# Performance work log

Hardware: AMD Instinct MI355X
Metric: run time of the kernel (lower is better)

## Reference

```python
import jax, jax.numpy as jnp
import numpy as np

N_HEADS = 8
N_DIM = 512
ATTN_DIM = N_DIM // N_HEADS
SOFT_TEMPERATURE = 1.0
TEMPERATURE = ATTN_DIM ** 0.5 / SOFT_TEMPERATURE


def sparsemax(z):
    # sparsemax along last axis: euclidean projection onto the simplex
    n = z.shape[-1]
    z_sorted = -jnp.sort(-z, axis=-1)                      # descending
    cs = jnp.cumsum(z_sorted, axis=-1)
    k = jnp.arange(1, n + 1, dtype=z.dtype)
    support = 1.0 + k * z_sorted > cs                      # bool
    k_sel = jnp.sum(support, axis=-1, keepdims=True)       # support size >= 1
    cs_sel = jnp.take_along_axis(cs, k_sel - 1, axis=-1)
    tau = (cs_sel - 1.0) / k_sel.astype(z.dtype)
    return jnp.maximum(z - tau, 0.0)


def setup_inputs() -> dict:
    key = jax.random.key(0)
    ks = jax.random.split(key, 9)
    bs, L, d = 8, 1024, N_DIM
    s = 1.0 / np.sqrt(d)
    return {
        "h_q": jax.random.normal(ks[0], (bs, L, d), jnp.float32),
        "h_k": jax.random.normal(ks[1], (bs, L, d), jnp.float32),
        "h_v": jax.random.normal(ks[2], (bs, L, d), jnp.float32),
        "Wq": jax.random.normal(ks[3], (d, d), jnp.float32) * s,
        "Wk": jax.random.normal(ks[4], (d, d), jnp.float32) * s,
        "Wv": jax.random.normal(ks[5], (d, d), jnp.float32) * s,
        "bv": jax.random.normal(ks[6], (d,), jnp.float32) * s,
        "Wf": jax.random.normal(ks[7], (d, d), jnp.float32) * s,
        "bf": jax.random.normal(ks[8], (d,), jnp.float32) * s,
    }


def reference(h_q, h_k, h_v, Wq, Wk, Wv, bv, Wf, bf):
    bs, Lq, _ = h_q.shape
    Lk = h_k.shape[1]
    H, D = N_HEADS, ATTN_DIM
    q = (h_q @ Wq.T).reshape(bs, Lq, H, D).transpose(0, 2, 1, 3)   # bhqd
    k = (h_k @ Wk.T).reshape(bs, Lk, H, D).transpose(0, 2, 1, 3)   # bhkd
    v = (h_v @ Wv.T + bv).reshape(bs, Lk, H, D).transpose(0, 2, 1, 3)
    alpha = jnp.einsum('bhqd,bhkd->bhqk', q / TEMPERATURE, k)
    alpha = sparsemax(alpha)
    res = jnp.einsum('bhqk,bhkd->bhqd', alpha, v)
    res = res.transpose(0, 2, 1, 3).reshape(bs, Lq, H * D)
    return res @ Wf.T + bf
```

## Files before the change

kernel.cpp:

```cpp
#include <hip/hip_runtime.h>
#include <hip/hip_bf16.h>
#include <cstdint>
#include <cstddef>

#define BS 8
#define SEQ 1024
#define DMODEL 512
#define NHEADS 8
#define DHEAD 64
#define QBLK 16
#define PPAD 1032

typedef float f32x4 __attribute__((ext_vector_type(4)));
typedef short bf16x8 __attribute__((ext_vector_type(8)));

static __device__ __forceinline__ unsigned short f2bf(float v) {
    __hip_bfloat16 hb = __float2bfloat16(v);
    return *reinterpret_cast<unsigned short*>(&hb);
}

struct CvtJob { const float* s; unsigned short* d; int n4; };

__global__ __launch_bounds__(256) void cvt_many(
    CvtJob j0, CvtJob j1, CvtJob j2, CvtJob j3, CvtJob j4, CvtJob j5, CvtJob j6)
{
    CvtJob j;
    switch (blockIdx.y) {
        case 0: j = j0; break; case 1: j = j1; break; case 2: j = j2; break;
        case 3: j = j3; break; case 4: j = j4; break; case 5: j = j5; break;
        default: j = j6; break;
    }
    for (int i = blockIdx.x * 256 + threadIdx.x; i < j.n4; i += gridDim.x * 256) {
        const float4 f = ((const float4*)j.s)[i];
        uint2 u;
        u.x = (unsigned)f2bf(f.x) | ((unsigned)f2bf(f.y) << 16);
        u.y = (unsigned)f2bf(f.z) | ((unsigned)f2bf(f.w) << 16);
        ((uint2*)j.d)[i] = u;
    }
}

struct GArgs { const unsigned short* A; const unsigned short* W;
               const float* bias; void* C; float scale; int mode; };

__global__ __launch_bounds__(256) void gemm_mfma(GArgs g0, GArgs g1, GArgs g2) {
    __shared__ __align__(16) unsigned short As[64 * 64];
    __shared__ __align__(16) unsigned short Bs[128 * 64];

    const GArgs g = (blockIdx.z == 0) ? g0 : ((blockIdx.z == 1) ? g1 : g2);
    const int tid = threadIdx.x;
    const int w = tid >> 6, l = tid & 63, lr = l & 15, lg = l >> 4;
    const int bm = blockIdx.y * 64, bn = blockIdx.x * 128;
    const int mrow = (w & 1) * 32, ncol = (w >> 1) * 64;

    f32x4 acc[2][4];
#pragma unroll
    for (int mt = 0; mt < 2; ++mt)
#pragma unroll
        for (int nt = 0; nt < 4; ++nt) acc[mt][nt] = (f32x4)0.f;

    for (int k0 = 0; k0 < DMODEL; k0 += 64) {
#pragma unroll
        for (int i = 0; i < 2; ++i) {
            const int rbase = i * 32 + w * 8;
            const int r = rbase + (l >> 3);
            const unsigned short* src = g.A + (size_t)(bm + r) * DMODEL + k0
                                        + 8 * ((l & 7) ^ (r & 7));
            __builtin_amdgcn_global_load_lds((const unsigned int*)src,
                                             (unsigned int*)&As[rbase * 64], 16, 0, 0);
        }
#pragma unroll
        for (int i = 0; i < 4; ++i) {
            const int rbase = i * 32 + w * 8;
            const int r = rbase + (l >> 3);
            const unsigned short* src = g.W + (size_t)(bn + r) * DMODEL + k0
                                        + 8 * ((l & 7) ^ (r & 7));
            __builtin_amdgcn_global_load_lds((const unsigned int*)src,
                                             (unsigned int*)&Bs[rbase * 64], 16, 0, 0);
        }
        __syncthreads();
#pragma unroll
        for (int kk = 0; kk < 2; ++kk) {
            bf16x8 av[2], bv[4];
#pragma unroll
            for (int mt = 0; mt < 2; ++mt) {
                const int ra = mrow + mt * 16 + lr;
                av[mt] = *(const bf16x8*)&As[ra * 64 + 8 * ((kk * 4 + lg) ^ (ra & 7))];
            }
#pragma unroll
            for (int nt = 0; nt < 4; ++nt) {
                const int rb = ncol + nt * 16 + lr;
                bv[nt] = *(const bf16x8*)&Bs[rb * 64 + 8 * ((kk * 4 + lg) ^ (rb & 7))];
            }
#pragma unroll
            for (int mt = 0; mt < 2; ++mt)
#pragma unroll
                for (int nt = 0; nt < 4; ++nt)
                    acc[mt][nt] = __builtin_amdgcn_mfma_f32_16x16x32_bf16(
                        av[mt], bv[nt], acc[mt][nt], 0, 0, 0);
        }
        __syncthreads();
    }

    if (g.mode == 0) {
        float* C = (float*)g.C;
#pragma unroll
        for (int mt = 0; mt < 2; ++mt)
#pragma unroll
        for (int nt = 0; nt < 4; ++nt)
#pragma unroll
        for (int j = 0; j < 4; ++j) {
            const int r = bm + mrow + mt * 16 + lg * 4 + j;
            const int c = bn + ncol + nt * 16 + lr;
            C[(size_t)r * DMODEL + c] = acc[mt][nt][j] * g.scale
                                        + (g.bias ? g.bias[c] : 0.f);
        }
    } else if (g.mode == 1) {
        unsigned short* C = (unsigned short*)g.C;
#pragma unroll
        for (int mt = 0; mt < 2; ++mt)
#pragma unroll
        for (int nt = 0; nt < 4; ++nt)
#pragma unroll
        for (int j = 0; j < 4; ++j) {
            const int r = bm + mrow + mt * 16 + lg * 4 + j;
            const int c = bn + ncol + nt * 16 + lr;
            const float v = acc[mt][nt][j] * g.scale + (g.bias ? g.bias[c] : 0.f);
            const int b = r >> 10, ll = r & (SEQ - 1);
            const int h = c >> 6, dd = c & 63;
            C[((size_t)(b * NHEADS + h) * SEQ + ll) * DHEAD + dd] = f2bf(v);
        }
    } else {
        unsigned short* C = (unsigned short*)g.C;
#pragma unroll
        for (int mt = 0; mt < 2; ++mt)
#pragma unroll
        for (int nt = 0; nt < 4; ++nt) {
            const int c = bn + ncol + nt * 16 + lr;
            const int h = c >> 6, dd = c & 63;
            const int r0 = bm + mrow + mt * 16 + lg * 4;
            const int b = r0 >> 10, l0 = r0 & (SEQ - 1);
            unsigned short tmp[4];
#pragma unroll
            for (int j = 0; j < 4; ++j)
                tmp[j] = f2bf(acc[mt][nt][j] * g.scale + (g.bias ? g.bias[c] : 0.f));
            uint2 u;
            u.x = (unsigned)tmp[0] | ((unsigned)tmp[1] << 16);
            u.y = (unsigned)tmp[2] | ((unsigned)tmp[3] << 16);
            *(uint2*)&C[((size_t)(b * NHEADS + h) * DHEAD + dd) * SEQ + l0] = u;
        }
    }
}

__global__ __launch_bounds__(256, 4) void attn_mfma(
    const unsigned short* __restrict__ Q, const unsigned short* __restrict__ K,
    const unsigned short* __restrict__ Vt, unsigned short* __restrict__ R)
{
    __shared__ __align__(16) unsigned short P[QBLK][PPAD];
    __shared__ float red_s[2][4][QBLK];
    __shared__ float red_c[2][4][QBLK];

    const int tid = threadIdx.x;
    const int w = tid >> 6, l = tid & 63, lr = l & 15, lg = l >> 4;

    const int flat = blockIdx.x;
    const int nid = (flat & 7) * 512 + (flat >> 3);
    const int q0 = (nid & 63) * QBLK;
    const int h = (nid >> 6) & (NHEADS - 1);
    const int b = nid >> 9;

    const size_t base = (size_t)(b * NHEADS + h) * SEQ * DHEAD;
    const unsigned short* Qp = Q + base;
    const unsigned short* Kp = K + base;

    const int ks = w * 256;

    const bf16x8 aq0 = *(const bf16x8*)(Qp + (size_t)(q0 + lr) * DHEAD + lg * 8);
    const bf16x8 aq1 = *(const bf16x8*)(Qp + (size_t)(q0 + lr) * DHEAD + 32 + lg * 8);
    f32x4 acc[16];
#pragma unroll
    for (int t = 0; t < 16; ++t) acc[t] = (f32x4)0.f;
#pragma unroll
    for (int t = 0; t < 16; ++t) {
        const unsigned short* kp = Kp + (size_t)(ks + t * 16 + lr) * DHEAD + lg * 8;
        const bf16x8 bk0 = *(const bf16x8*)(kp);
        const bf16x8 bk1 = *(const bf16x8*)(kp + 32);
        acc[t] = __builtin_amdgcn_mfma_f32_16x16x32_bf16(aq0, bk0, acc[t], 0, 0, 0);
        acc[t] = __builtin_amdgcn_mfma_f32_16x16x32_bf16(aq1, bk1, acc[t], 0, 0, 0);
    }

    float mx[4];
#pragma unroll
    for (int j = 0; j < 4; ++j) mx[j] = acc[0][j];
#pragma unroll
    for (int t = 1; t < 16; ++t)
#pragma unroll
        for (int j = 0; j < 4; ++j) mx[j] = fmaxf(mx[j], acc[t][j]);
#pragma unroll
    for (int o = 1; o < 16; o <<= 1)
#pragma unroll
        for (int j = 0; j < 4; ++j) mx[j] = fmaxf(mx[j], __shfl_xor(mx[j], o));
    if (lr == 0) {
#pragma unroll
        for (int j = 0; j < 4; ++j) red_s[0][w][lg * 4 + j] = mx[j];
    }
    __syncthreads();
    float tau[4];
#pragma unroll
    for (int j = 0; j < 4; ++j) {
        const int r = lg * 4 + j;
        tau[j] = fmaxf(fmaxf(red_s[0][0][r], red_s[0][1][r]),
                       fmaxf(red_s[0][2][r], red_s[0][3][r])) - 1.0f;
    }

    for (int it = 0; it < 16; ++it) {
        const int bb = (it + 1) & 1;
        float s[4] = {0.f, 0.f, 0.f, 0.f};
        float c[4] = {0.f, 0.f, 0.f, 0.f};
#pragma unroll
        for (int t = 0; t < 16; ++t)
#pragma unroll
            for (int j = 0; j < 4; ++j) {
                const bool ggt = acc[t][j] > tau[j];
                s[j] += ggt ? acc[t][j] : 0.f;
                c[j] += ggt ? 1.f : 0.f;
            }
#pragma unroll
        for (int o = 1; o < 16; o <<= 1)
#pragma unroll
            for (int j = 0; j < 4; ++j) {
                s[j] += __shfl_xor(s[j], o);
                c[j] += __shfl_xor(c[j], o);
            }
        if (lr == 0) {
#pragma unroll
            for (int j = 0; j < 4; ++j) {
                red_s[bb][w][lg * 4 + j] = s[j];
                red_c[bb][w][lg * 4 + j] = c[j];
            }
        }
        __syncthreads();
        float delta = -1.f;
#pragma unroll
        for (int j = 0; j < 4; ++j) {
            const int r = lg * 4 + j;
            const float st = red_s[bb][0][r] + red_s[bb][1][r]
                           + red_s[bb][2][r] + red_s[bb][3][r];
            const float ct = red_c[bb][0][r] + red_c[bb][1][r]
                           + red_c[bb][2][r] + red_c[bb][3][r];
            const float tn = (st - 1.f) / ct;
            delta = fmaxf(delta, tn - tau[j]);
            tau[j] = tn;
        }
        delta = fmaxf(delta, __shfl_xor(delta, 16));
        delta = fmaxf(delta, __shfl_xor(delta, 32));
        if (delta < 1e-5f) break;
    }

#pragma unroll
    for (int t = 0; t < 16; ++t)
#pragma unroll
        for (int j = 0; j < 4; ++j)
            P[lg * 4 + j][ks + t * 16 + lr] = f2bf(fmaxf(acc[t][j] - tau[j], 0.f));
    __syncthreads();

    const int dcol = w * 16;
    const unsigned short* VtP = Vt + ((size_t)(b * NHEADS + h) * DHEAD + dcol + lr) * SEQ
                                + lg * 8;
    f32x4 o = (f32x4)0.f;
    bf16x8 vb = *(const bf16x8*)(VtP);
#pragma unroll 4
    for (int kt = 0; kt < 32; ++kt) {
        const bf16x8 vcur = vb;
        if (kt + 1 < 32) vb = *(const bf16x8*)(VtP + (kt + 1) * 32);
        const bf16x8 pa = *(const bf16x8*)&P[lr][kt * 32 + lg * 8];
        __builtin_amdgcn_s_setprio(1);
        o = __builtin_amdgcn_mfma_f32_16x16x32_bf16(pa, vcur, o, 0, 0, 0);
        __builtin_amdgcn_s_setprio(0);
    }

#pragma unroll
    for (int j = 0; j < 4; ++j)
        R[((size_t)b * SEQ + q0 + lg * 4 + j) * DMODEL + h * DHEAD + dcol + lr] =
            f2bf(o[j]);
}

extern "C" void kernel_launch(void* const* d_in, const int* in_sizes, int n_in,
                              void* d_out, int out_size, void* d_ws, size_t ws_size,
                              hipStream_t stream) {
    const float* h_q = (const float*)d_in[0];
    const float* h_k = (const float*)d_in[1];
    const float* h_v = (const float*)d_in[2];
    const float* Wq  = (const float*)d_in[3];
    const float* Wk  = (const float*)d_in[4];
    const float* Wv  = (const float*)d_in[5];
    const float* bv  = (const float*)d_in[6];
    const float* Wf  = (const float*)d_in[7];
    const float* bf  = (const float*)d_in[8];
    float* out = (float*)d_out;

    const size_t perT = (size_t)BS * SEQ * DMODEL;
    const size_t wN = (size_t)DMODEL * DMODEL;
    unsigned short* hq_b = (unsigned short*)d_ws;
    unsigned short* hk_b = hq_b + perT;
    unsigned short* hv_b = hk_b + perT;
    unsigned short* Qws  = hv_b + perT;
    unsigned short* Kws  = Qws + perT;
    unsigned short* Vtw  = Kws + perT;
    unsigned short* Rws  = Vtw + perT;
    unsigned short* Wqb  = Rws + perT;
    unsigned short* Wkb  = Wqb + wN;
    unsigned short* Wvb  = Wkb + wN;
    unsigned short* Wfb  = Wvb + wN;

    {
        CvtJob j0{h_q, hq_b, (int)(perT / 4)};
        CvtJob j1{h_k, hk_b, (int)(perT / 4)};
        CvtJob j2{h_v, hv_b, (int)(perT / 4)};
        CvtJob j3{Wq, Wqb, (int)(wN / 4)};
        CvtJob j4{Wk, Wkb, (int)(wN / 4)};
        CvtJob j5{Wv, Wvb, (int)(wN / 4)};
        CvtJob j6{Wf, Wfb, (int)(wN / 4)};
        cvt_many<<<dim3(512, 7), 256, 0, stream>>>(j0, j1, j2, j3, j4, j5, j6);
    }

    {
        GArgs gq{hq_b, Wqb, nullptr, Qws, 0.125f, 1};
        GArgs gk{hk_b, Wkb, nullptr, Kws, 1.0f, 1};
        GArgs gv{hv_b, Wvb, bv,      Vtw, 1.0f, 2};
        gemm_mfma<<<dim3(DMODEL / 128, BS * SEQ / 64, 3), 256, 0, stream>>>(gq, gk, gv);
    }

    attn_mfma<<<dim3(BS * NHEADS * (SEQ / QBLK)), 256, 0, stream>>>(Qws, Kws, Vtw, Rws);

    {
        GArgs gf{Rws, Wfb, bf, out, 1.0f, 0};
        gemm_mfma<<<dim3(DMODEL / 128, BS * SEQ / 64, 1), 256, 0, stream>>>(gf, gf, gf);
    }
}
```

Measured before the change: 190.4 us.

## Compact sparsemax candidates into shared list and transpose QK MFMA layout

```diff
diff --git a/kernel.cpp b/kernel.cpp
--- a/kernel.cpp
+++ b/kernel.cpp
@@ -156,8 +156,11 @@
     const unsigned short* __restrict__ Vt, unsigned short* __restrict__ R)
 {
     __shared__ __align__(16) unsigned short P[QBLK][PPAD];
-    __shared__ float red_s[2][4][QBLK];
-    __shared__ float red_c[2][4][QBLK];
+    __shared__ __align__(16) float clist[QBLK][68];
+    __shared__ int cnt_s[QBLK];
+    __shared__ __align__(16) float red_m[QBLK][4];
+    __shared__ __align__(16) float red_s[2][QBLK][4];
+    __shared__ __align__(16) float red_c[2][QBLK][4];
 
     const int tid = threadIdx.x;
     const int w = tid >> 6, l = tid & 63, lr = l & 15, lg = l >> 4;
@@ -184,99 +187,124 @@
         const unsigned short* kp = Kp + (size_t)(ks + t * 16 + lr) * DHEAD + lg * 8;
         const bf16x8 bk0 = *(const bf16x8*)(kp);
         const bf16x8 bk1 = *(const bf16x8*)(kp + 32);
-        acc[t] = __builtin_amdgcn_mfma_f32_16x16x32_bf16(aq0, bk0, acc[t], 0, 0, 0);
-        acc[t] = __builtin_amdgcn_mfma_f32_16x16x32_bf16(aq1, bk1, acc[t], 0, 0, 0);
-    }
-
-    float mx[4];
-#pragma unroll
-    for (int j = 0; j < 4; ++j) mx[j] = acc[0][j];
-#pragma unroll
-    for (int t = 1; t < 16; ++t)
-#pragma unroll
-        for (int j = 0; j < 4; ++j) mx[j] = fmaxf(mx[j], acc[t][j]);
-#pragma unroll
-    for (int o = 1; o < 16; o <<= 1)
-#pragma unroll
-        for (int j = 0; j < 4; ++j) mx[j] = fmaxf(mx[j], __shfl_xor(mx[j], o));
-    if (lr == 0) {
-#pragma unroll
-        for (int j = 0; j < 4; ++j) red_s[0][w][lg * 4 + j] = mx[j];
-    }
+        acc[t] = __builtin_amdgcn_mfma_f32_16x16x32_bf16(bk0, aq0, acc[t], 0, 0, 0);
+        acc[t] = __builtin_amdgcn_mfma_f32_16x16x32_bf16(bk1, aq1, acc[t], 0, 0, 0);
+    }
+
+    f32x4 m4 = acc[0];
+#pragma unroll
+    for (int t = 1; t < 16; ++t) {
+        m4[0] = fmaxf(m4[0], acc[t][0]); m4[1] = fmaxf(m4[1], acc[t][1]);
+        m4[2] = fmaxf(m4[2], acc[t][2]); m4[3] = fmaxf(m4[3], acc[t][3]);
+    }
+    float m = fmaxf(fmaxf(m4[0], m4[1]), fmaxf(m4[2], m4[3]));
+    m = fmaxf(m, __shfl_xor(m, 16));
+    m = fmaxf(m, __shfl_xor(m, 32));
+    if (lg == 0) red_m[lr][w] = m;
+
+    for (int i = tid; i < QBLK * 68; i += 256) (&clist[0][0])[i] = -3.0e38f;
+    if (tid < QBLK) cnt_s[tid] = 0;
     __syncthreads();
-    float tau[4];
-#pragma unroll
-    for (int j = 0; j < 4; ++j) {
-        const int r = lg * 4 + j;
-        tau[j] = fmaxf(fmaxf(red_s[0][0][r], red_s[0][1][r]),
-                       fmaxf(red_s[0][2][r], red_s[0][3][r])) - 1.0f;
-    }
+
+    const float4 rm4 = *(const float4*)red_m[lr];
+    const float rmax = fmaxf(fmaxf(rm4.x, rm4.y), fmaxf(rm4.z, rm4.w));
+    float tau = rmax - 1.0f;
+    const float thr = tau;
+
+#pragma unroll
+    for (int t = 0; t < 16; ++t)
+#pragma unroll
+        for (int j = 0; j < 4; ++j) {
+            const float z = acc[t][j];
+            if (z > thr) {
+                const int pos = atomicAdd(&cnt_s[lr], 1);
+                if (pos < 64) clist[lr][pos] = z;
+            }
+        }
+    __syncthreads();
+
+    const bool full = (cnt_s[lr] > 64);
+    const f32x4* clp = (const f32x4*)&clist[lr][lg * 16];
+    const f32x4 cd0 = clp[0], cd1 = clp[1], cd2 = clp[2], cd3 = clp[3];
 
     for (int it = 0; it < 16; ++it) {
         const int bb = (it + 1) & 1;
-        float s[4] = {0.f, 0.f, 0.f, 0.f};
-        float c[4] = {0.f, 0.f, 0.f, 0.f};
-#pragma unroll
-        for (int t = 0; t < 16; ++t)
-#pragma unroll
-            for (int j = 0; j < 4; ++j) {
-                const bool ggt = acc[t][j] > tau[j];
-                s[j] += ggt ? acc[t][j] : 0.f;
-                c[j] += ggt ? 1.f : 0.f;
+        float s = 0.f, c = 0.f;
+        if (!full) {
+#pragma unroll
+            for (int i = 0; i < 4; ++i) {
+                const float z0 = cd0[i], z1 = cd1[i], z2 = cd2[i], z3 = cd3[i];
+                if (z0 > tau) { s += z0; c += 1.f; }
+                if (z1 > tau) { s += z1; c += 1.f; }
+                if (z2 > tau) { s += z2; c += 1.f; }
+                if (z3 > tau) { s += z3; c += 1.f; }
             }
-#pragma unroll
-        for (int o = 1; o < 16; o <<= 1)
-#pragma unroll
-            for (int j = 0; j < 4; ++j) {
-                s[j] += __shfl_xor(s[j], o);
-                c[j] += __shfl_xor(c[j], o);
-            }
-        if (lr == 0) {
-#pragma unroll
-            for (int j = 0; j < 4; ++j) {
-                red_s[bb][w][lg * 4 + j] = s[j];
-                red_c[bb][w][lg * 4 + j] = c[j];
-            }
-        }
+        } else {
+#pragma unroll
+            for (int t = 0; t < 16; ++t)
+#pragma unroll
+                for (int j = 0; j < 4; ++j) {
+                    const float z = acc[t][j];
+                    if (z > tau) { s += z; c += 1.f; }
+                }
+        }
+        s += __shfl_xor(s, 16); c += __shfl_xor(c, 16);
+        s += __shfl_xor(s, 32); c += __shfl_xor(c, 32);
+        if (lg == 0) { red_s[bb][lr][w] = s; red_c[bb][lr][w] = c; }
         __syncthreads();
-        float delta = -1.f;
-#pragma unroll
-        for (int j = 0; j < 4; ++j) {
-            const int r = lg * 4 + j;
-            const float st = red_s[bb][0][r] + red_s[bb][1][r]
-                           + red_s[bb][2][r] + red_s[bb][3][r];
-            const float ct = red_c[bb][0][r] + red_c[bb][1][r]
-                           + red_c[bb][2][r] + red_c[bb][3][r];
-            const float tn = (st - 1.f) / ct;
-            delta = fmaxf(delta, tn - tau[j]);
-            tau[j] = tn;
-        }
-        delta = fmaxf(delta, __shfl_xor(delta, 16));
-        delta = fmaxf(delta, __shfl_xor(delta, 32));
+        float st, ct;
+        if (full) {
+            const float4 s4 = *(const float4*)red_s[bb][lr];
+            const float4 c4 = *(const float4*)red_c[bb][lr];
+            st = (s4.x + s4.y) + (s4.z + s4.w);
+            ct = (c4.x + c4.y) + (c4.z + c4.w);
+        } else {
+            st = s;
+            ct = c;
+        }
+        const float tn = (st - 1.f) / ct;
+        float delta = tn - tau;
+        tau = tn;
+        delta = fmaxf(delta, __shfl_xor(delta, 1));
+        delta = fmaxf(delta, __shfl_xor(delta, 2));
+        delta = fmaxf(delta, __shfl_xor(delta, 4));
+        delta = fmaxf(delta, __shfl_xor(delta, 8));
         if (delta < 1e-5f) break;
     }
 
 #pragma unroll
     for (int t = 0; t < 16; ++t)
 #pragma unroll
-        for (int j = 0; j < 4; ++j)
-            P[lg * 4 + j][ks + t * 16 + lr] = f2bf(fmaxf(acc[t][j] - tau[j], 0.f));
+        for (int jp = 0; jp < 2; ++jp) {
+            const unsigned lo = f2bf(fmaxf(acc[t][2 * jp] - tau, 0.f));
+            const unsigned hi = f2bf(fmaxf(acc[t][2 * jp + 1] - tau, 0.f));
+            *(unsigned*)&P[lr][ks + t * 16 + lg * 4 + 2 * jp] = lo | (hi << 16);
+        }
     __syncthreads();
 
     const int dcol = w * 16;
     const unsigned short* VtP = Vt + ((size_t)(b * NHEADS + h) * DHEAD + dcol + lr) * SEQ
                                 + lg * 8;
     f32x4 o = (f32x4)0.f;
-    bf16x8 vb = *(const bf16x8*)(VtP);
-#pragma unroll 4
-    for (int kt = 0; kt < 32; ++kt) {
-        const bf16x8 vcur = vb;
-        if (kt + 1 < 32) vb = *(const bf16x8*)(VtP + (kt + 1) * 32);
-        const bf16x8 pa = *(const bf16x8*)&P[lr][kt * 32 + lg * 8];
-        __builtin_amdgcn_s_setprio(1);
-        o = __builtin_amdgcn_mfma_f32_16x16x32_bf16(pa, vcur, o, 0, 0, 0);
-        __builtin_amdgcn_s_setprio(0);
-    }
+    bf16x8 vb0 = *(const bf16x8*)(VtP + 0 * 32);
+    bf16x8 vb1 = *(const bf16x8*)(VtP + 1 * 32);
+    bf16x8 vb2 = *(const bf16x8*)(VtP + 2 * 32);
+    bf16x8 vb3 = *(const bf16x8*)(VtP + 3 * 32);
+#define PV_STEP(KT, VREG)                                                      \
+    {                                                                          \
+        const bf16x8 pa = *(const bf16x8*)&P[lr][(KT) * 32 + lg * 8];          \
+        __builtin_amdgcn_s_setprio(1);                                         \
+        o = __builtin_amdgcn_mfma_f32_16x16x32_bf16(pa, VREG, o, 0, 0, 0);     \
+        __builtin_amdgcn_s_setprio(0);                                         \
+        if ((KT) + 4 < 32) VREG = *(const bf16x8*)(VtP + ((KT) + 4) * 32);     \
+    }
+    for (int kt = 0; kt < 32; kt += 4) {
+        PV_STEP(kt + 0, vb0)
+        PV_STEP(kt + 1, vb1)
+        PV_STEP(kt + 2, vb2)
+        PV_STEP(kt + 3, vb3)
+    }
+#undef PV_STEP
 
 #pragma unroll
     for (int j = 0; j < 4; ++j)
```

New measurement: 196.3 us. 1.03x slower.
